# Optimization experiments

Measured on AMD Instinct MI355X. Metric: run time of the kernel, lower is better.

## Reference

```python
import jax, jax.numpy as jnp
import numpy as np

N_HEAD = 16
D_MODEL = 1024
D_K = 64
D_V = 64
B = 8
L = 1024
EPS = 1e-5
NEG_INF = -1e9


def setup_inputs() -> dict:
    key = jax.random.key(0)
    ks = jax.random.split(key, 6)
    qkv_out = N_HEAD * (2 * D_K + D_V)  # 3072
    x = jax.random.normal(ks[0], (B, L, D_MODEL), dtype=jnp.float32)
    # causal attention mask (N, 1, L, L), 1 = keep, 0 = masked
    mask = jnp.broadcast_to(jnp.tril(jnp.ones((L, L), jnp.float32))[None, None], (B, 1, L, L))
    W_qkv = jax.random.normal(ks[1], (D_MODEL, qkv_out), dtype=jnp.float32) * 0.02
    b_qkv = jnp.zeros((qkv_out,), jnp.float32)
    W_proj = jax.random.normal(ks[2], (N_HEAD * D_V, D_MODEL), dtype=jnp.float32) * 0.02
    b_proj = jnp.zeros((D_MODEL,), jnp.float32)
    gamma = jnp.ones((D_MODEL,), jnp.float32)
    beta = jnp.zeros((D_MODEL,), jnp.float32)
    return {"x": x, "mask": mask, "W_qkv": W_qkv, "b_qkv": b_qkv,
            "W_proj": W_proj, "b_proj": b_proj, "gamma": gamma, "beta": beta}


def _layer_norm(x, gamma, beta):
    u = jnp.mean(x, axis=-1, keepdims=True)
    s = jnp.mean(jnp.square(x - u), axis=-1, keepdims=True)
    return gamma * (x - u) / jnp.sqrt(s + EPS) + beta


def reference(x, mask, W_qkv, b_qkv, W_proj, b_proj, gamma, beta):
    residual = x
    qkv = jnp.einsum('bld,df->blf', x, W_qkv) + b_qkv  # 1x1 Conv1D == pointwise linear
    q_l = N_HEAD * D_K
    q = qkv[:, :, :q_l]
    k = qkv[:, :, q_l:2 * q_l]
    v = qkv[:, :, 2 * q_l:]
    # split heads: (B, L, H*D) -> (B, H, L, D)
    q = q.reshape(B, L, N_HEAD, D_K).transpose(0, 2, 1, 3)
    k = k.reshape(B, L, N_HEAD, D_K).transpose(0, 2, 1, 3)
    v = v.reshape(B, L, N_HEAD, D_V).transpose(0, 2, 1, 3)
    temperature = np.power(D_K, 0.5)
    attn = jnp.einsum('bhqd,bhkd->bhqk', q, k) / temperature
    attn = mask * attn + (1.0 - mask) * NEG_INF
    attn = jax.nn.softmax(attn, axis=-1)  # dropout is identity in eval mode
    out = jnp.einsum('bhqk,bhkd->bhqd', attn, v)
    # merge heads: (B, H, L, Dv) -> (B, L, H*Dv)
    out = out.transpose(0, 2, 1, 3).reshape(B, L, N_HEAD * D_V)
    out = jnp.einsum('blf,fd->bld', out, W_proj) + b_proj
    out = _layer_norm(out + residual, gamma, beta)
    return out, attn
```

## Files before the change

### kernel.cpp

```cpp
#include <hip/hip_runtime.h>

typedef __attribute__((ext_vector_type(4))) float f32x4;
typedef __attribute__((ext_vector_type(8))) __bf16 bf16x8;
typedef __attribute__((ext_vector_type(8))) unsigned short ushort8;

static __device__ __forceinline__ unsigned short f2bf(float f) {
    unsigned int u = __float_as_uint(f);
    u += 0x7fffu + ((u >> 16) & 1u);
    return (unsigned short)(u >> 16);
}
static __device__ __forceinline__ float bf2f(unsigned short u) {
    return __uint_as_float((unsigned int)u << 16);
}
static __device__ __forceinline__ bf16x8 as_bf(ushort8 v) {
    union { ushort8 u; bf16x8 b; } x; x.u = v; return x.b;
}
static __device__ __forceinline__ void gll16(const void* g, void* l) {
    __builtin_amdgcn_global_load_lds(
        (const __attribute__((address_space(1))) void*)g,
        (__attribute__((address_space(3))) void*)l, 16, 0, 0);
}

__global__ void cvt_bf16(const float* __restrict__ in, unsigned short* __restrict__ out,
                         int n8) {
    int i = blockIdx.x * 256 + threadIdx.x;
    if (i >= n8) return;
    const float4* p = (const float4*)(in + (size_t)i * 8);
    float4 a = p[0], b = p[1];
    ushort8 o = { f2bf(a.x), f2bf(a.y), f2bf(a.z), f2bf(a.w),
                  f2bf(b.x), f2bf(b.y), f2bf(b.z), f2bf(b.w) };
    *(ushort8*)(out + (size_t)i * 8) = o;
}

__global__ void tconv_bf16(const float* __restrict__ in, unsigned short* __restrict__ out,
                           int K, int N) {
    __shared__ float t[64][65];
    const int tid = threadIdx.x;
    const int n0 = blockIdx.x * 64, k0 = blockIdx.y * 64;
#pragma unroll
    for (int i = 0; i < 4; i++) {
        int idx = tid + 256 * i;
        int r = idx >> 4, c4 = (idx & 15) * 4;
        float4 v = *(const float4*)(in + (size_t)(k0 + r) * N + n0 + c4);
        t[r][c4] = v.x; t[r][c4 + 1] = v.y; t[r][c4 + 2] = v.z; t[r][c4 + 3] = v.w;
    }
    __syncthreads();
#pragma unroll
    for (int i = 0; i < 2; i++) {
        int idx = tid + 256 * i;
        int nl = idx >> 3, k8 = (idx & 7) * 8;
        ushort8 o;
#pragma unroll
        for (int j = 0; j < 8; j++) o[j] = f2bf(t[k8 + j][nl]);
        *(ushort8*)(out + (size_t)(n0 + nl) * K + k0 + k8) = o;
    }
}

template <int EPI>
__global__ __launch_bounds__(256, 2)
void gemm_bf16(const unsigned short* __restrict__ A,
               const unsigned short* __restrict__ BT,
               const float* __restrict__ bias,
               unsigned short* __restrict__ qh, unsigned short* __restrict__ kh,
               unsigned short* __restrict__ vh,
               float* __restrict__ Cf,
               int K, int mtiles, int Ncols)
{
    __shared__ unsigned short smem[2 * 128 * 64];
    unsigned short* As = smem;
    unsigned short* Bs = smem + 128 * 64;

    const int tid = threadIdx.x;
    const int wid = tid >> 6, lane = tid & 63;
    const int g = lane >> 4, c = lane & 15;
    const int wr = (wid >> 1) * 64, wc = (wid & 1) * 64;

    const int nwg = gridDim.x;
    const int swz = ((int)blockIdx.x & 7) * (nwg >> 3) + ((int)blockIdx.x >> 3);
    const int bm = (swz % mtiles) * 128;
    const int bn = (swz / mtiles) * 128;

    const int srow = lane >> 3;
    const int scol8 = ((lane & 7) ^ srow) * 8;
    const size_t arow0 = (size_t)(bm + wid * 8 + srow);
    const size_t brow0 = (size_t)(bn + wid * 8 + srow);

    f32x4 acc[4][4] = {};

    for (int k0 = 0; k0 < K; k0 += 64) {
        __syncthreads();
#pragma unroll
        for (int t = 0; t < 4; t++) {
            gll16(A + (arow0 + t * 32) * K + k0 + scol8,
                  (char*)As + t * 4096 + wid * 1024);
            gll16(BT + (brow0 + t * 32) * K + k0 + scol8,
                  (char*)Bs + t * 4096 + wid * 1024);
        }
        __syncthreads();
#pragma unroll
        for (int ks = 0; ks < 2; ks++) {
            bf16x8 af[4], bfr[4];
#pragma unroll
            for (int mi = 0; mi < 4; mi++) {
                int row = wr + mi * 16 + c;
                int off = row * 128 + ((ks * 64 + g * 16) ^ ((c & 7) << 4));
                af[mi] = as_bf(*(const ushort8*)((const char*)As + off));
            }
#pragma unroll
            for (int ni = 0; ni < 4; ni++) {
                int row = wc + ni * 16 + c;
                int off = row * 128 + ((ks * 64 + g * 16) ^ ((c & 7) << 4));
                bfr[ni] = as_bf(*(const ushort8*)((const char*)Bs + off));
            }
#pragma unroll
            for (int mi = 0; mi < 4; mi++)
#pragma unroll
                for (int ni = 0; ni < 4; ni++)
                    acc[mi][ni] = __builtin_amdgcn_mfma_f32_16x16x32_bf16(
                        af[mi], bfr[ni], acc[mi][ni], 0, 0, 0);
        }
    }

    if (EPI == 1) {
#pragma unroll
        for (int mi = 0; mi < 4; mi++)
#pragma unroll
            for (int ni = 0; ni < 4; ni++)
#pragma unroll
                for (int r = 0; r < 4; r++) {
                    int m = bm + wr + mi * 16 + g * 4 + r;
                    int n = bn + wc + ni * 16 + c;
                    Cf[(size_t)m * Ncols + n] = acc[mi][ni][r] + bias[n];
                }
    } else {
#pragma unroll
        for (int nh = 0; nh < 2; nh++) {
            __syncthreads();
            if ((wid & 1) == nh) {
#pragma unroll
                for (int mi = 0; mi < 4; mi++)
#pragma unroll
                    for (int ni = 0; ni < 4; ni++)
#pragma unroll
                        for (int r = 0; r < 4; r++) {
                            int row = wr + mi * 16 + g * 4 + r;
                            int col = ni * 16 + c;
                            float v = acc[mi][ni][r] + bias[bn + nh * 64 + col];
                            smem[row * 64 + col] = f2bf(v);
                        }
            }
            __syncthreads();
            int n0 = bn + nh * 64;
            int region = n0 >> 10;
            int h = (n0 & 1023) >> 6;
            unsigned short* dst = region == 0 ? qh : region == 1 ? kh : vh;
#pragma unroll
            for (int i = 0; i < 4; i++) {
                int idx = tid + 256 * i;
                int row = idx >> 3, c8 = (idx & 7) * 8;
                ushort8 v = *(const ushort8*)&smem[row * 64 + c8];
                int m = bm + row;
                int b = m >> 10, l = m & 1023;
                *(ushort8*)(dst + ((size_t)((b * 16 + h) * 1024 + l)) * 64 + c8) = v;
            }
        }
    }
}

__global__ __launch_bounds__(256, 2)
void attn_kernel(const unsigned short* __restrict__ qh,
                 const unsigned short* __restrict__ kh,
                 const unsigned short* __restrict__ vh,
                 float* __restrict__ attn, unsigned short* __restrict__ ob)
{
    const int bh = blockIdx.x;
    const int qt = blockIdx.y;
    const int tid = threadIdx.x, wid = tid >> 6, lane = tid & 63;
    const int g = lane >> 4, c = lane & 15;
    const int q0 = qt * 64;

    __shared__ unsigned short Ks[64 * 64];
    __shared__ unsigned short Vt[64 * 64];
    __shared__ unsigned short Ps[4 * 1024];

    const size_t baseKV = (size_t)bh * (1024 * 64);

    const int qrow = q0 + wid * 16 + c;
    bf16x8 qa[2];
    qa[0] = as_bf(*(const ushort8*)(qh + baseKV + (size_t)qrow * 64 + g * 8));
    qa[1] = as_bf(*(const ushort8*)(qh + baseKV + (size_t)qrow * 64 + 32 + g * 8));

    const int srow = lane >> 3;
    const int scol8 = ((lane & 7) ^ srow) * 8;

    float mrow[4], lrow[4];
#pragma unroll
    for (int r = 0; r < 4; r++) { mrow[r] = -INFINITY; lrow[r] = 0.f; }
    const float scale = 0.125f;

    for (int kt = 0; kt <= qt; ++kt) {
        const unsigned short* kb = kh + baseKV + (size_t)kt * 4096;
        __syncthreads();
        gll16(kb + (size_t)(wid * 8 + srow) * 64 + scol8, (char*)Ks + wid * 1024);
        gll16(kb + (size_t)(32 + wid * 8 + srow) * 64 + scol8, (char*)Ks + 4096 + wid * 1024);
        __syncthreads();

        f32x4 s[4];
#pragma unroll
        for (int ni = 0; ni < 4; ni++) {
            f32x4 a = {0.f, 0.f, 0.f, 0.f};
            int krow = ni * 16 + c;
#pragma unroll
            for (int ks = 0; ks < 2; ks++) {
                int off = krow * 128 + ((ks * 64 + g * 16) ^ ((krow & 7) << 4));
                bf16x8 kf = as_bf(*(const ushort8*)((const char*)Ks + off));
                a = __builtin_amdgcn_mfma_f32_16x16x32_bf16(qa[ks], kf, a, 0, 0, 0);
            }
            s[ni] = a;
        }
#pragma unroll
        for (int ni = 0; ni < 4; ni++) {
            int kcol = kt * 64 + ni * 16 + c;
#pragma unroll
            for (int r = 0; r < 4; r++) {
                int qr = q0 + wid * 16 + g * 4 + r;
                float v = s[ni][r] * scale;
                s[ni][r] = (kcol > qr) ? -1e9f : v;
            }
        }
#pragma unroll
        for (int r = 0; r < 4; r++) {
            float mx = fmaxf(fmaxf(s[0][r], s[1][r]), fmaxf(s[2][r], s[3][r]));
#pragma unroll
            for (int d = 1; d < 16; d <<= 1) mx = fmaxf(mx, __shfl_xor(mx, d));
            float nm = fmaxf(mrow[r], mx);
            float sum = __expf(s[0][r] - nm) + __expf(s[1][r] - nm) +
                        __expf(s[2][r] - nm) + __expf(s[3][r] - nm);
#pragma unroll
            for (int d = 1; d < 16; d <<= 1) sum += __shfl_xor(sum, d);
            lrow[r] = lrow[r] * __expf(mrow[r] - nm) + sum;
            mrow[r] = nm;
        }
    }
    float rinv[4];
#pragma unroll
    for (int r = 0; r < 4; r++) rinv[r] = 1.f / lrow[r];

    f32x4 oacc[4] = {};
    float* attnB = attn + (size_t)bh * (1024 * 1024);
    for (int kt = 0; kt <= qt; ++kt) {
        const unsigned short* kb = kh + baseKV + (size_t)kt * 4096;
        const unsigned short* vb = vh + baseKV + (size_t)kt * 4096;
        __syncthreads();
        gll16(kb + (size_t)(wid * 8 + srow) * 64 + scol8, (char*)Ks + wid * 1024);
        gll16(kb + (size_t)(32 + wid * 8 + srow) * 64 + scol8, (char*)Ks + 4096 + wid * 1024);
#pragma unroll
        for (int i = 0; i < 2; i++) {
            int cidx = tid + 256 * i;
            int row = cidx >> 3, col16 = cidx & 7;
            ushort8 v = *(const ushort8*)(vb + (size_t)row * 64 + col16 * 8);
#pragma unroll
            for (int j = 0; j < 8; j++) {
                int d = col16 * 8 + j;
                int off = d * 128 + ((row * 2) ^ ((d & 7) << 4));
                *(unsigned short*)((char*)Vt + off) = v[j];
            }
        }
        __syncthreads();

        f32x4 s[4];
#pragma unroll
        for (int ni = 0; ni < 4; ni++) {
            f32x4 a = {0.f, 0.f, 0.f, 0.f};
            int krow = ni * 16 + c;
#pragma unroll
            for (int ks = 0; ks < 2; ks++) {
                int off = krow * 128 + ((ks * 64 + g * 16) ^ ((krow & 7) << 4));
                bf16x8 kf = as_bf(*(const ushort8*)((const char*)Ks + off));
                a = __builtin_amdgcn_mfma_f32_16x16x32_bf16(qa[ks], kf, a, 0, 0, 0);
            }
            s[ni] = a;
        }
#pragma unroll
        for (int ni = 0; ni < 4; ni++) {
            int kcol = kt * 64 + ni * 16 + c;
#pragma unroll
            for (int r = 0; r < 4; r++) {
                int qlr = g * 4 + r;
                int qr = q0 + wid * 16 + qlr;
                float sv = (kcol > qr) ? -1e9f : s[ni][r] * scale;
                float p = __expf(sv - mrow[r]) * rinv[r];
                int pcol = ni * 16 + c;
                int off = wid * 2048 + qlr * 128 + ((pcol * 2) ^ ((qlr & 7) << 4));
                *(unsigned short*)((char*)Ps + off) = f2bf(p);
            }
        }
#pragma unroll
        for (int ks = 0; ks < 2; ks++) {
            int aoff = wid * 2048 + c * 128 + ((ks * 64 + g * 16) ^ ((c & 7) << 4));
            bf16x8 pa = as_bf(*(const ushort8*)((const char*)Ps + aoff));
#pragma unroll
            for (int ni = 0; ni < 4; ni++) {
                int d = ni * 16 + c;
                int voff = d * 128 + ((ks * 64 + g * 16) ^ ((d & 7) << 4));
                bf16x8 vf = as_bf(*(const ushort8*)((const char*)Vt + voff));
                oacc[ni] = __builtin_amdgcn_mfma_f32_16x16x32_bf16(pa, vf, oacc[ni], 0, 0, 0);
            }
        }
        __syncthreads();
#pragma unroll
        for (int i = 0; i < 2; i++) {
            int idx = tid + 256 * i;
            int row = idx >> 3, c16 = idx & 7;
            int off = (row >> 4) * 2048 + (row & 15) * 128 + ((c16 * 16) ^ ((row & 7) << 4));
            ushort8 v = *(const ushort8*)((const char*)Ps + off);
            float4 f0 = { bf2f(v[0]), bf2f(v[1]), bf2f(v[2]), bf2f(v[3]) };
            float4 f1 = { bf2f(v[4]), bf2f(v[5]), bf2f(v[6]), bf2f(v[7]) };
            float* dp = attnB + (size_t)(q0 + row) * 1024 + kt * 64 + c16 * 8;
            *(float4*)dp = f0;
            *(float4*)(dp + 4) = f1;
        }
    }

    {
        float4 z = {0.f, 0.f, 0.f, 0.f};
        float* zb = attnB + (size_t)q0 * 1024;
        for (int kt = qt + 1; kt < 16; ++kt) {
#pragma unroll
            for (int i = 0; i < 4; i++) {
                int idx = tid + 256 * i;
                int row = idx >> 4, c4 = (idx & 15) << 2;
                *(float4*)(zb + (size_t)row * 1024 + kt * 64 + c4) = z;
            }
        }
    }

    __syncthreads();
#pragma unroll
    for (int ni = 0; ni < 4; ni++)
#pragma unroll
        for (int r = 0; r < 4; r++) {
            int row = wid * 16 + g * 4 + r;
            int d = ni * 16 + c;
            int off = row * 128 + ((d * 2) ^ ((row & 7) << 4));
            *(unsigned short*)((char*)Ks + off) = f2bf(oacc[ni][r]);
        }
    __syncthreads();
    {
        const int b = bh >> 4, h = bh & 15;
#pragma unroll
        for (int i = 0; i < 2; i++) {
            int idx = tid + 256 * i;
            int row = idx >> 3, c16 = idx & 7;
            int off = row * 128 + ((c16 * 16) ^ ((row & 7) << 4));
            ushort8 v = *(const ushort8*)((const char*)Ks + off);
            *(ushort8*)(ob + ((size_t)(b * 1024 + q0 + row)) * 1024 + h * 64 + c16 * 8) = v;
        }
    }
}

__global__ __launch_bounds__(256, 2)
void ln_kernel(const float* __restrict__ y, const float* __restrict__ x,
               const float* __restrict__ gamma, const float* __restrict__ beta,
               float* __restrict__ out)
{
    const int m = blockIdx.x;
    const int tid = threadIdx.x;
    const int wid = tid >> 6, lane = tid & 63;
    float4 vy = *(const float4*)(y + (size_t)m * 1024 + tid * 4);
    float4 vx = *(const float4*)(x + (size_t)m * 1024 + tid * 4);
    float4 v = {vy.x + vx.x, vy.y + vx.y, vy.z + vx.z, vy.w + vx.w};
    float s1 = v.x + v.y + v.z + v.w;
    float s2 = v.x * v.x + v.y * v.y + v.z * v.z + v.w * v.w;
#pragma unroll
    for (int d = 1; d < 64; d <<= 1) {
        s1 += __shfl_xor(s1, d);
        s2 += __shfl_xor(s2, d);
    }
    __shared__ float red1[4], red2[4];
    if (lane == 0) { red1[wid] = s1; red2[wid] = s2; }
    __syncthreads();
    float t1 = red1[0] + red1[1] + red1[2] + red1[3];
    float t2 = red2[0] + red2[1] + red2[2] + red2[3];
    float mean = t1 * (1.f / 1024.f);
    float var = t2 * (1.f / 1024.f) - mean * mean;
    float rstd = rsqrtf(var + 1e-5f);
    float4 g4 = *(const float4*)(gamma + tid * 4);
    float4 b4 = *(const float4*)(beta + tid * 4);
    float4 o;
    o.x = g4.x * (v.x - mean) * rstd + b4.x;
    o.y = g4.y * (v.y - mean) * rstd + b4.y;
    o.z = g4.z * (v.z - mean) * rstd + b4.z;
    o.w = g4.w * (v.w - mean) * rstd + b4.w;
    *(float4*)(out + (size_t)m * 1024 + tid * 4) = o;
}

extern "C" void kernel_launch(void* const* d_in, const int* in_sizes, int n_in,
                              void* d_out, int out_size, void* d_ws, size_t ws_size,
                              hipStream_t stream)
{
    const float* x      = (const float*)d_in[0];
    const float* W_qkv  = (const float*)d_in[2];
    const float* b_qkv  = (const float*)d_in[3];
    const float* W_proj = (const float*)d_in[4];
    const float* b_proj = (const float*)d_in[5];
    const float* gamma  = (const float*)d_in[6];
    const float* beta   = (const float*)d_in[7];

    float* out  = (float*)d_out;
    float* attn = out + (size_t)8 * 1024 * 1024;

    const size_t E = (size_t)8192 * 1024;
    unsigned short* ws = (unsigned short*)d_ws;
    unsigned short* qh     = ws;
    unsigned short* kh     = qh + E;
    unsigned short* vh     = kh + E;
    unsigned short* xb     = vh + E;
    unsigned short* wqkvT  = xb + E;
    unsigned short* wprojT = wqkvT + (size_t)3072 * 1024;
    unsigned short* ob     = wprojT + (size_t)1024 * 1024;
    float* yb = (float*)(void*)qh;

    cvt_bf16<<<4096, 256, 0, stream>>>(x, xb, (int)(E / 8));
    tconv_bf16<<<dim3(48, 16), 256, 0, stream>>>(W_qkv, wqkvT, 1024, 3072);
    tconv_bf16<<<dim3(16, 16), 256, 0, stream>>>(W_proj, wprojT, 1024, 1024);

    gemm_bf16<0><<<1536, 256, 0, stream>>>(xb, wqkvT, b_qkv,
                                           qh, kh, vh, nullptr, 1024, 64, 3072);
    attn_kernel<<<dim3(128, 16), 256, 0, stream>>>(qh, kh, vh, attn, ob);
    gemm_bf16<1><<<512, 256, 0, stream>>>(ob, wprojT, b_proj,
                                          nullptr, nullptr, nullptr, yb, 1024, 64, 1024);
    ln_kernel<<<8192, 256, 0, stream>>>(yb, x, gamma, beta, out);
}
```

Baseline: 304.2 us.

## Make attention single-pass: buffer unnormalized P in LDS, normalize at write-out

The attention kernel no longer makes a separate pass to find the softmax max and sum. Each block handles 32 query rows and computes exp(scores) without subtracting a max. It keeps the whole unnormalized bf16 probability row in 64KB of dynamic LDS and accumulates row sums. The keys of each tile are split across two warp groups, whose partial outputs and sums are merged through LDS. The attn matrix, including its zeros, is then written once in fp32 with the normalization applied. This drops the duplicate QK^T pass, at the cost of 80KB of LDS per block (lower occupancy) and possible overflow if scores are large, since the max is no longer subtracted.

```diff
diff --git a/kernel.cpp b/kernel.cpp
--- a/kernel.cpp
+++ b/kernel.cpp
@@ -173,19 +173,27 @@
                  const unsigned short* __restrict__ vh,
                  float* __restrict__ attn, unsigned short* __restrict__ ob)
 {
-    const int bh = blockIdx.x;
-    const int qt = blockIdx.y;
+    extern __shared__ char smem[];
+    char* Ks = smem + 65536;
+    char* Vt = smem + 73728;
+    float* lS    = (float*)(smem + 65536);
+    float* rinvS = (float*)(smem + 65664);
+    unsigned short* Obf = (unsigned short*)(smem + 65792);
+    float* Ot    = (float*)(smem + 73728);
+
+    const int qt = blockIdx.x;
+    const int bh = blockIdx.y;
+    const int q0 = qt * 32;
+    const int ntiles = (qt >> 1) + 1;
+
     const int tid = threadIdx.x, wid = tid >> 6, lane = tid & 63;
     const int g = lane >> 4, c = lane & 15;
-    const int q0 = qt * 64;
-
-    __shared__ unsigned short Ks[64 * 64];
-    __shared__ unsigned short Vt[64 * 64];
-    __shared__ unsigned short Ps[4 * 1024];
+    const int rowblk = wid & 1;
+    const int grp = wid >> 1;
 
     const size_t baseKV = (size_t)bh * (1024 * 64);
 
-    const int qrow = q0 + wid * 16 + c;
+    const int qrow = q0 + rowblk * 16 + c;
     bf16x8 qa[2];
     qa[0] = as_bf(*(const ushort8*)(qh + baseKV + (size_t)qrow * 64 + g * 8));
     qa[1] = as_bf(*(const ushort8*)(qh + baseKV + (size_t)qrow * 64 + 32 + g * 8));
@@ -193,67 +201,15 @@
     const int srow = lane >> 3;
     const int scol8 = ((lane & 7) ^ srow) * 8;
 
-    float mrow[4], lrow[4];
-#pragma unroll
-    for (int r = 0; r < 4; r++) { mrow[r] = -INFINITY; lrow[r] = 0.f; }
-    const float scale = 0.125f;
-
-    for (int kt = 0; kt <= qt; ++kt) {
-        const unsigned short* kb = kh + baseKV + (size_t)kt * 4096;
-        __syncthreads();
-        gll16(kb + (size_t)(wid * 8 + srow) * 64 + scol8, (char*)Ks + wid * 1024);
-        gll16(kb + (size_t)(32 + wid * 8 + srow) * 64 + scol8, (char*)Ks + 4096 + wid * 1024);
-        __syncthreads();
-
-        f32x4 s[4];
-#pragma unroll
-        for (int ni = 0; ni < 4; ni++) {
-            f32x4 a = {0.f, 0.f, 0.f, 0.f};
-            int krow = ni * 16 + c;
-#pragma unroll
-            for (int ks = 0; ks < 2; ks++) {
-                int off = krow * 128 + ((ks * 64 + g * 16) ^ ((krow & 7) << 4));
-                bf16x8 kf = as_bf(*(const ushort8*)((const char*)Ks + off));
-                a = __builtin_amdgcn_mfma_f32_16x16x32_bf16(qa[ks], kf, a, 0, 0, 0);
-            }
-            s[ni] = a;
-        }
-#pragma unroll
-        for (int ni = 0; ni < 4; ni++) {
-            int kcol = kt * 64 + ni * 16 + c;
-#pragma unroll
-            for (int r = 0; r < 4; r++) {
-                int qr = q0 + wid * 16 + g * 4 + r;
-                float v = s[ni][r] * scale;
-                s[ni][r] = (kcol > qr) ? -1e9f : v;
-            }
-        }
-#pragma unroll
-        for (int r = 0; r < 4; r++) {
-            float mx = fmaxf(fmaxf(s[0][r], s[1][r]), fmaxf(s[2][r], s[3][r]));
-#pragma unroll
-            for (int d = 1; d < 16; d <<= 1) mx = fmaxf(mx, __shfl_xor(mx, d));
-            float nm = fmaxf(mrow[r], mx);
-            float sum = __expf(s[0][r] - nm) + __expf(s[1][r] - nm) +
-                        __expf(s[2][r] - nm) + __expf(s[3][r] - nm);
-#pragma unroll
-            for (int d = 1; d < 16; d <<= 1) sum += __shfl_xor(sum, d);
-            lrow[r] = lrow[r] * __expf(mrow[r] - nm) + sum;
-            mrow[r] = nm;
-        }
-    }
-    float rinv[4];
-#pragma unroll
-    for (int r = 0; r < 4; r++) rinv[r] = 1.f / lrow[r];
-
+    float lpart[4] = {0.f, 0.f, 0.f, 0.f};
     f32x4 oacc[4] = {};
-    float* attnB = attn + (size_t)bh * (1024 * 1024);
-    for (int kt = 0; kt <= qt; ++kt) {
+
+    for (int kt = 0; kt < ntiles; ++kt) {
         const unsigned short* kb = kh + baseKV + (size_t)kt * 4096;
         const unsigned short* vb = vh + baseKV + (size_t)kt * 4096;
         __syncthreads();
-        gll16(kb + (size_t)(wid * 8 + srow) * 64 + scol8, (char*)Ks + wid * 1024);
-        gll16(kb + (size_t)(32 + wid * 8 + srow) * 64 + scol8, (char*)Ks + 4096 + wid * 1024);
+        gll16(kb + (size_t)(wid * 8 + srow) * 64 + scol8, Ks + wid * 1024);
+        gll16(kb + (size_t)(32 + wid * 8 + srow) * 64 + scol8, Ks + 4096 + wid * 1024);
 #pragma unroll
         for (int i = 0; i < 2; i++) {
             int cidx = tid + 256 * i;
@@ -263,98 +219,112 @@
             for (int j = 0; j < 8; j++) {
                 int d = col16 * 8 + j;
                 int off = d * 128 + ((row * 2) ^ ((d & 7) << 4));
-                *(unsigned short*)((char*)Vt + off) = v[j];
+                *(unsigned short*)(Vt + off) = v[j];
             }
         }
         __syncthreads();
 
-        f32x4 s[4];
-#pragma unroll
-        for (int ni = 0; ni < 4; ni++) {
+        f32x4 s[2];
+#pragma unroll
+        for (int ni = 0; ni < 2; ni++) {
             f32x4 a = {0.f, 0.f, 0.f, 0.f};
-            int krow = ni * 16 + c;
+            int krow = grp * 32 + ni * 16 + c;
 #pragma unroll
             for (int ks = 0; ks < 2; ks++) {
                 int off = krow * 128 + ((ks * 64 + g * 16) ^ ((krow & 7) << 4));
-                bf16x8 kf = as_bf(*(const ushort8*)((const char*)Ks + off));
+                bf16x8 kf = as_bf(*(const ushort8*)(Ks + off));
                 a = __builtin_amdgcn_mfma_f32_16x16x32_bf16(qa[ks], kf, a, 0, 0, 0);
             }
             s[ni] = a;
         }
 #pragma unroll
-        for (int ni = 0; ni < 4; ni++) {
-            int kcol = kt * 64 + ni * 16 + c;
+        for (int ni = 0; ni < 2; ni++) {
+            int kcol = kt * 64 + grp * 32 + ni * 16 + c;
 #pragma unroll
             for (int r = 0; r < 4; r++) {
-                int qlr = g * 4 + r;
-                int qr = q0 + wid * 16 + qlr;
-                float sv = (kcol > qr) ? -1e9f : s[ni][r] * scale;
-                float p = __expf(sv - mrow[r]) * rinv[r];
-                int pcol = ni * 16 + c;
-                int off = wid * 2048 + qlr * 128 + ((pcol * 2) ^ ((qlr & 7) << 4));
-                *(unsigned short*)((char*)Ps + off) = f2bf(p);
-            }
-        }
-#pragma unroll
-        for (int ks = 0; ks < 2; ks++) {
-            int aoff = wid * 2048 + c * 128 + ((ks * 64 + g * 16) ^ ((c & 7) << 4));
-            bf16x8 pa = as_bf(*(const ushort8*)((const char*)Ps + aoff));
+                int prow = rowblk * 16 + g * 4 + r;
+                int qr = q0 + prow;
+                float p = (kcol > qr) ? 0.f : __expf(s[ni][r] * 0.125f);
+                lpart[r] += p;
+                int off = prow * 2048 + ((kcol * 2) ^ ((prow & 7) << 4));
+                *(unsigned short*)(smem + off) = f2bf(p);
+            }
+        }
+        {
+            int prowA = rowblk * 16 + c;
+            int aoff = prowA * 2048 +
+                       (((kt * 64 + grp * 32 + g * 8) * 2) ^ ((prowA & 7) << 4));
+            bf16x8 pa = as_bf(*(const ushort8*)(smem + aoff));
 #pragma unroll
             for (int ni = 0; ni < 4; ni++) {
                 int d = ni * 16 + c;
-                int voff = d * 128 + ((ks * 64 + g * 16) ^ ((d & 7) << 4));
-                bf16x8 vf = as_bf(*(const ushort8*)((const char*)Vt + voff));
+                int voff = d * 128 + (((grp * 32 + g * 8) * 2) ^ ((d & 7) << 4));
+                bf16x8 vf = as_bf(*(const ushort8*)(Vt + voff));
                 oacc[ni] = __builtin_amdgcn_mfma_f32_16x16x32_bf16(pa, vf, oacc[ni], 0, 0, 0);
             }
         }
-        __syncthreads();
-#pragma unroll
-        for (int i = 0; i < 2; i++) {
-            int idx = tid + 256 * i;
-            int row = idx >> 3, c16 = idx & 7;
-            int off = (row >> 4) * 2048 + (row & 15) * 128 + ((c16 * 16) ^ ((row & 7) << 4));
-            ushort8 v = *(const ushort8*)((const char*)Ps + off);
-            float4 f0 = { bf2f(v[0]), bf2f(v[1]), bf2f(v[2]), bf2f(v[3]) };
-            float4 f1 = { bf2f(v[4]), bf2f(v[5]), bf2f(v[6]), bf2f(v[7]) };
-            float* dp = attnB + (size_t)(q0 + row) * 1024 + kt * 64 + c16 * 8;
-            *(float4*)dp = f0;
-            *(float4*)(dp + 4) = f1;
-        }
-    }
-
-    {
-        float4 z = {0.f, 0.f, 0.f, 0.f};
-        float* zb = attnB + (size_t)q0 * 1024;
-        for (int kt = qt + 1; kt < 16; ++kt) {
-#pragma unroll
-            for (int i = 0; i < 4; i++) {
-                int idx = tid + 256 * i;
-                int row = idx >> 4, c4 = (idx & 15) << 2;
-                *(float4*)(zb + (size_t)row * 1024 + kt * 64 + c4) = z;
-            }
-        }
-    }
+    }
+
+#pragma unroll
+    for (int r = 0; r < 4; r++)
+#pragma unroll
+        for (int d = 1; d < 16; d <<= 1) lpart[r] += __shfl_xor(lpart[r], d);
 
     __syncthreads();
-#pragma unroll
-    for (int ni = 0; ni < 4; ni++)
+    if (grp == 1) {
+        if (c == 0) {
+#pragma unroll
+            for (int r = 0; r < 4; r++) lS[rowblk * 16 + g * 4 + r] = lpart[r];
+        }
+#pragma unroll
+        for (int ni = 0; ni < 4; ni++)
+#pragma unroll
+            for (int r = 0; r < 4; r++)
+                Ot[(rowblk * 16 + g * 4 + r) * 64 + ni * 16 + c] = oacc[ni][r];
+    }
+    __syncthreads();
+    if (grp == 0) {
+        float rinv[4];
 #pragma unroll
         for (int r = 0; r < 4; r++) {
-            int row = wid * 16 + g * 4 + r;
-            int d = ni * 16 + c;
-            int off = row * 128 + ((d * 2) ^ ((row & 7) << 4));
-            *(unsigned short*)((char*)Ks + off) = f2bf(oacc[ni][r]);
-        }
+            int row = rowblk * 16 + g * 4 + r;
+            rinv[r] = 1.f / (lpart[r] + lS[row]);
+            if (c == 0) rinvS[row] = rinv[r];
+        }
+#pragma unroll
+        for (int ni = 0; ni < 4; ni++)
+#pragma unroll
+            for (int r = 0; r < 4; r++) {
+                int row = rowblk * 16 + g * 4 + r;
+                int d = ni * 16 + c;
+                float o = (oacc[ni][r] + Ot[row * 64 + d]) * rinv[r];
+                Obf[row * 64 + d] = f2bf(o);
+            }
+    }
     __syncthreads();
+
     {
         const int b = bh >> 4, h = bh & 15;
-#pragma unroll
-        for (int i = 0; i < 2; i++) {
-            int idx = tid + 256 * i;
-            int row = idx >> 3, c16 = idx & 7;
-            int off = row * 128 + ((c16 * 16) ^ ((row & 7) << 4));
-            ushort8 v = *(const ushort8*)((const char*)Ks + off);
-            *(ushort8*)(ob + ((size_t)(b * 1024 + q0 + row)) * 1024 + h * 64 + c16 * 8) = v;
+        int row = tid >> 3, c8 = tid & 7;
+        ushort8 v = *(const ushort8*)&Obf[row * 64 + c8 * 8];
+        *(ushort8*)(ob + ((size_t)(b * 1024 + q0 + row)) * 1024 + h * 64 + c8 * 8) = v;
+    }
+
+    {
+        float* attnB = attn + (size_t)bh * (1024 * 1024) + (size_t)q0 * 1024;
+        const int maxcol = ntiles * 64;
+        const bool live = (tid * 4) < maxcol;
+#pragma unroll 4
+        for (int row = 0; row < 32; ++row) {
+            float4 o = {0.f, 0.f, 0.f, 0.f};
+            if (live) {
+                float rinv = rinvS[row];
+                int off = row * 2048 + ((tid * 8) ^ ((row & 7) << 4));
+                ushort4 u = *(const ushort4*)(smem + off);
+                o.x = bf2f(u.x) * rinv; o.y = bf2f(u.y) * rinv;
+                o.z = bf2f(u.z) * rinv; o.w = bf2f(u.w) * rinv;
+            }
+            *(float4*)(attnB + (size_t)row * 1024 + tid * 4) = o;
         }
     }
 }
@@ -427,7 +397,7 @@
 
     gemm_bf16<0><<<1536, 256, 0, stream>>>(xb, wqkvT, b_qkv,
                                            qh, kh, vh, nullptr, 1024, 64, 3072);
-    attn_kernel<<<dim3(128, 16), 256, 0, stream>>>(qh, kh, vh, attn, ob);
+    attn_kernel<<<dim3(32, 128), 256, 81920, stream>>>(qh, kh, vh, attn, ob);
     gemm_bf16<1><<<512, 256, 0, stream>>>(ob, wprojT, b_proj,
                                           nullptr, nullptr, nullptr, yb, 1024, 64, 1024);
     ln_kernel<<<8192, 256, 0, stream>>>(yb, x, gamma, beta, out);
```

Result: slower. 395.0 us (+29.8%).
